# Kernel optimization log

Hardware: AMD Instinct MI355X
Metric: run time of the kernel (lower is better)

Reference implementation:

```python
import jax, jax.numpy as jnp
import numpy as np

N = 100000          # nodes
E = 1600000         # edges (avg degree 16)
IN_F = 256          # in_features
OUT_F = 128         # out_features


def setup_inputs() -> dict:
    key = jax.random.key(0)
    k1, k2, k3, k4, k5 = jax.random.split(key, 5)
    x = jax.random.normal(k1, (N, IN_F), dtype=jnp.float32)
    edge_index = jax.random.randint(k2, (2, E), 0, N, dtype=jnp.int32)
    # xavier_uniform-style init (gain 1.414)
    def xav(k, shape):
        fan_in, fan_out = shape[0], shape[1]
        bound = 1.414 * np.sqrt(6.0 / (fan_in + fan_out))
        return jax.random.uniform(k, shape, jnp.float32, -bound, bound)
    W = xav(k3, (IN_F, OUT_F))
    a = xav(k4, (2 * OUT_F, 1))
    W_em = xav(k5, (IN_F, OUT_F))
    return {"x": x, "edge_index": edge_index, "W": W, "a": a, "W_em": W_em}


def reference(x, edge_index, W, a, W_em):
    # DisGALayer.forward_sparse, att_type=1, gnn_type='AT', eval mode (dropout off)
    src = edge_index[0]
    dst = edge_index[1]
    h = x @ W                                   # [N, OUT_F]
    # edge_e = cat(h[src], h[dst]) @ a  ==  h[src]@a_src + h[dst]@a_dst
    a_src, a_dst = a[:OUT_F], a[OUT_F:]
    edge_e = h[src] @ a_src + h[dst] @ a_dst    # [E, 1]
    edge_ob = jax.nn.sigmoid(edge_e)            # [E, 1]
    # sp_softmax: softmax of edge values grouped by row (src)
    v = jnp.exp(edge_ob - jax.lax.stop_gradient(edge_ob.max()))
    denom = jax.ops.segment_sum(v, src, num_segments=N)   # [N, 1]
    attention = v / denom[src]                  # [E, 1]
    # sp_matmul: h_prime[i] = sum_{e: src(e)=i} att_e * h_em[dst(e)]
    h_em = x @ W_em                             # [N, OUT_F]
    h_prime = jax.ops.segment_sum(attention * h_em[dst], src, num_segments=N)
    return h_prime, edge_e
```

## Files before the change

kernel.cpp:

```cpp
#include <hip/hip_runtime.h>
#include <hip/hip_bf16.h>

#define NN 100000
#define NE 1600000
#define INF 256
#define OUTF 128
#define NBK ((NN + 127) / 128)
#define CHUNK 4096
#define NBA ((NE + CHUNK - 1) / CHUNK)
#define NGRP (NN / 32)
#define SCAP 6144
#define NMM 1563

#define GLOBAL_AS __attribute__((address_space(1)))
#define LDS_AS __attribute__((address_space(3)))

typedef __attribute__((ext_vector_type(8))) short short8;
typedef __attribute__((ext_vector_type(4))) float f32x4;

static __device__ __forceinline__ short f2bf(float f) {
    __hip_bfloat16 h = __float2bfloat16(f);
    return *reinterpret_cast<short*>(&h);
}

__global__ void k_setup(const float* __restrict__ W, const float* __restrict__ a,
                        const float* __restrict__ Wem, const int* __restrict__ src,
                        float* __restrict__ wsv, float* __restrict__ wdv,
                        ushort* __restrict__ Bsw, int* __restrict__ cntA) {
    const int b = blockIdx.x, t = threadIdx.x;
    if (b == 0) {
        const float* Wr = W + (size_t)t * OUTF;
        float sa = 0.f, sb = 0.f;
        #pragma unroll 8
        for (int k = 0; k < OUTF; ++k) {
            float w = Wr[k];
            sa += w * a[k];
            sb += w * a[OUTF + k];
        }
        wsv[t] = sa;
        wdv[t] = sb;
    } else if (b <= 8) {
        const int kt = b - 1;
        for (int idx = t; idx < 4096; idx += 256) {
            const int ct = idx >> 9;
            const int lane = (idx >> 3) & 63;
            const int j = idx & 7;
            const int k = kt * 32 + (lane >> 4) * 8 + j;
            const int c = ct * 16 + (lane & 15);
            Bsw[((size_t)(kt * 8 + ct) * 64 + lane) * 8 + j] =
                (ushort)f2bf(Wem[(size_t)k * OUTF + c]);
        }
    } else {
        __shared__ int cnt[NBK];
        const int c = b - 9;
        const int e0 = c * CHUNK;
        for (int i = t; i < NBK; i += 256) cnt[i] = 0;
        __syncthreads();
        for (int i = t; i < CHUNK; i += 256) {
            const int e = e0 + i;
            if (e < NE) atomicAdd(&cnt[src[e] >> 7], 1);
        }
        __syncthreads();
        for (int i = t; i < NBK; i += 256) cntA[(size_t)c * NBK + i] = cnt[i];
    }
}

__global__ __launch_bounds__(256) void k_mmcs(
    const float* __restrict__ x, const ushort* __restrict__ Bsw,
    const float* __restrict__ wsv, const float* __restrict__ wdv,
    const int* __restrict__ cntA,
    float* __restrict__ s1, float* __restrict__ s2,
    char* __restrict__ hem8, float* __restrict__ scaleA,
    int* __restrict__ baseA, int* __restrict__ bsumB) {
    __shared__ float xs[64 * 256];
    __shared__ int sm[512];
    const int b = blockIdx.x;
    const int t = threadIdx.x;
    if (b < NMM) {
        const int w = t >> 6, lane = t & 63;
        const int rowbase = b * 64 + w * 16;
        const int r0 = lane & 15, kq = lane >> 4;

        #pragma unroll
        for (int it = 0; it < 16; ++it) {
            const int r = w * 16 + it;
            const int gr = b * 64 + r;
            const int grc = (gr < NN) ? gr : NN - 1;
            const int chunk = lane ^ (r & 15);
            const float* gsrc = x + (size_t)grc * INF + chunk * 4;
            __builtin_amdgcn_global_load_lds(
                (const GLOBAL_AS uint*)gsrc,
                (LDS_AS uint*)&xs[r * 256], 16, 0, 0);
        }
        __syncthreads();

        const float* xrow = &xs[(size_t)(w * 16 + r0) * 256];
        const short8* bp = reinterpret_cast<const short8*>(Bsw);
        f32x4 acc[8];
        #pragma unroll
        for (int ct = 0; ct < 8; ++ct) acc[ct] = (f32x4){0.f, 0.f, 0.f, 0.f};
        float sa = 0.f, sb = 0.f;

        #pragma unroll
        for (int kt = 0; kt < 8; ++kt) {
            const int c0 = kt * 8 + kq * 2;
            const float4 a0 = *reinterpret_cast<const float4*>(
                xrow + ((c0 ^ r0) << 2));
            const float4 a1 = *reinterpret_cast<const float4*>(
                xrow + (((c0 + 1) ^ r0) << 2));
            const float4 w0 = *reinterpret_cast<const float4*>(wsv + kt * 32 + kq * 8);
            const float4 w1 = *reinterpret_cast<const float4*>(wsv + kt * 32 + kq * 8 + 4);
            const float4 u0 = *reinterpret_cast<const float4*>(wdv + kt * 32 + kq * 8);
            const float4 u1 = *reinterpret_cast<const float4*>(wdv + kt * 32 + kq * 8 + 4);
            sa += a0.x * w0.x + a0.y * w0.y + a0.z * w0.z + a0.w * w0.w
                + a1.x * w1.x + a1.y * w1.y + a1.z * w1.z + a1.w * w1.w;
            sb += a0.x * u0.x + a0.y * u0.y + a0.z * u0.z + a0.w * u0.w
                + a1.x * u1.x + a1.y * u1.y + a1.z * u1.z + a1.w * u1.w;
            short8 af;
            af[0] = f2bf(a0.x); af[1] = f2bf(a0.y); af[2] = f2bf(a0.z); af[3] = f2bf(a0.w);
            af[4] = f2bf(a1.x); af[5] = f2bf(a1.y); af[6] = f2bf(a1.z); af[7] = f2bf(a1.w);
            #pragma unroll
            for (int ct = 0; ct < 8; ++ct) {
                const short8 bf = bp[(size_t)(kt * 8 + ct) * 64 + lane];
                acc[ct] = __builtin_amdgcn_mfma_f32_16x16x32_bf16(af, bf, acc[ct], 0, 0, 0);
            }
        }

        sa += __shfl_xor(sa, 16); sa += __shfl_xor(sa, 32);
        sb += __shfl_xor(sb, 16); sb += __shfl_xor(sb, 32);
        const int row = rowbase + r0;
        if (kq == 0 && row < NN) { s1[row] = sa; s2[row] = sb; }

        float mx[4];
        #pragma unroll
        for (int i = 0; i < 4; ++i) {
            float m = 0.f;
            #pragma unroll
            for (int ct = 0; ct < 8; ++ct) m = fmaxf(m, fabsf(acc[ct][i]));
            m = fmaxf(m, __shfl_xor(m, 1));
            m = fmaxf(m, __shfl_xor(m, 2));
            m = fmaxf(m, __shfl_xor(m, 4));
            m = fmaxf(m, __shfl_xor(m, 8));
            mx[i] = m;
        }
        #pragma unroll
        for (int i = 0; i < 4; ++i) {
            const int rr = rowbase + kq * 4 + i;
            const float inv = (mx[i] > 0.f) ? 127.f / mx[i] : 0.f;
            if (r0 == 0 && rr < NN) scaleA[rr] = mx[i];
            #pragma unroll
            for (int ct = 0; ct < 8; ++ct) {
                int q = (int)rintf(acc[ct][i] * inv);
                q = (q > 127) ? 127 : ((q < -127) ? -127 : q);
                uint p = (uint)(q & 255);
                p |= ((uint)__shfl_xor((int)p, 1) & 255u) << 8;
                uint word = p | ((uint)__shfl_xor((int)p, 2) << 16);
                if ((r0 & 3) == 0 && rr < NN) {
                    *reinterpret_cast<uint*>(
                        hem8 + ((size_t)(ct >> 1) * NN + rr) * 32
                             + (ct & 1) * 16 + r0) = word;
                }
            }
        }
    } else {
        const int bb = b - NMM;
        const int v0 = (t < NBA) ? cntA[(size_t)t * NBK + bb] : 0;
        const int t2 = t + 256;
        const int v1 = (t2 < NBA) ? cntA[(size_t)t2 * NBK + bb] : 0;
        sm[t] = v0;
        sm[t2] = v1;
        __syncthreads();
        for (int off = 1; off < 512; off <<= 1) {
            const int a0 = (t >= off) ? sm[t - off] : 0;
            const int a1 = (t2 >= off) ? sm[t2 - off] : 0;
            __syncthreads();
            sm[t] += a0;
            sm[t2] += a1;
            __syncthreads();
        }
        if (t < NBA) baseA[(size_t)t * NBK + bb] = sm[t] - v0;
        if (t2 < NBA) baseA[(size_t)t2 * NBK + bb] = sm[t2] - v1;
        if (t == 255) bsumB[bb] = sm[511];
    }
}

__global__ __launch_bounds__(1024) void k_bbase(
    const int* __restrict__ bsumB, int* __restrict__ bbase,
    int* __restrict__ offs) {
    __shared__ int sm[1024];
    const int t = threadIdx.x;
    const int v = (t < NBK) ? bsumB[t] : 0;
    sm[t] = v;
    __syncthreads();
    for (int off = 1; off < 1024; off <<= 1) {
        const int add = (t >= off) ? sm[t - off] : 0;
        __syncthreads();
        sm[t] += add;
        __syncthreads();
    }
    if (t < NBK) bbase[t] = sm[t] - v;
    if (t == 0) { bbase[NBK] = NE; offs[NN] = NE; }
}

__global__ __launch_bounds__(256) void k_binA(
    const int* __restrict__ src, const int* __restrict__ dst,
    const float* __restrict__ s1, const float* __restrict__ s2,
    float* __restrict__ ee_out, const int* __restrict__ bbase,
    const int* __restrict__ baseA, int2* __restrict__ ebA) {
    __shared__ int base[NBK];
    __shared__ int cnt[NBK];
    const int t = threadIdx.x;
    const int c = blockIdx.x;
    const int e0 = c * CHUNK;
    for (int i = t; i < NBK; i += 256) {
        base[i] = bbase[i] + baseA[(size_t)c * NBK + i];
        cnt[i] = 0;
    }
    __syncthreads();
    for (int i = t; i < CHUNK; i += 256) {
        const int e = e0 + i;
        if (e < NE) {
            const int s = src[e], d = dst[e];
            const float ee = s1[s] + s2[d];
            __builtin_nontemporal_store(ee, ee_out + e);
            const float ob = 1.f / (1.f + __expf(-ee));
            const float v = __expf(ob);
            int vq = (int)((v - 1.f) * 16384.f + 0.5f);
            vq = (vq > 32767) ? 32767 : vq;
            const int bk = s >> 7;
            const int r = atomicAdd(&cnt[bk], 1);
            ebA[base[bk] + r] = make_int2((d << 7) | (s & 127), vq);
        }
    }
}

__global__ __launch_bounds__(256) void k_sortB(
    const int* __restrict__ bbase, const int2* __restrict__ ebA,
    const float* __restrict__ scaleA,
    uint* __restrict__ ebB, int* __restrict__ offs) {
    __shared__ uint rx[SCAP];
    __shared__ ushort ry[SCAP];
    __shared__ int cnt[128];
    __shared__ int sum[128];
    __shared__ int sm[128];
    __shared__ int cur[128];
    __shared__ float fsl[128];
    const int b = blockIdx.x, t = threadIdx.x;
    const int n0 = b << 7;
    const int lo = bbase[b];
    const int hi = bbase[b + 1];
    const int n = hi - lo;
    if (t < 128) { cnt[t] = 0; sum[t] = 0; }
    __syncthreads();
    for (int i = t; i < n; i += 256) {
        const int2 r = ebA[lo + i];
        if (i < SCAP) { rx[i] = (uint)r.x; ry[i] = (ushort)r.y; }
        const int sidx = r.x & 127;
        atomicAdd(&cnt[sidx], 1);
        atomicAdd(&sum[sidx], r.y);
    }
    __syncthreads();
    const int v = (t < 128) ? cnt[t] : 0;
    if (t < 128) sm[t] = v;
    __syncthreads();
    for (int off = 1; off < 128; off <<= 1) {
        int add = 0;
        if (t < 128 && t >= off) add = sm[t - off];
        __syncthreads();
        if (t < 128) sm[t] += add;
        __syncthreads();
    }
    if (t < 128) {
        const int excl = sm[t] - v;
        cur[t] = excl;
        const int node = n0 + t;
        if (node < NN) offs[node] = lo + excl;
        fsl[t] = (v > 0) ? 1.f / (float)(v * 16384 + sum[t]) : 0.f;
    }
    __syncthreads();
    for (int i = t; i < n; i += 256) {
        uint x;
        int y;
        if (i < SCAP) { x = rx[i]; y = (int)ry[i]; }
        else { const int2 r = ebA[lo + i]; x = (uint)r.x; y = r.y; }
        const int sidx = x & 127;
        const uint d = x >> 7;
        const float att = (float)(16384 + y) * fsl[sidx];
        const float w = att * scaleA[d];
        int wq = (int)(w * 1024.f + 0.5f);
        wq = (wq > 32767) ? 32767 : wq;
        const int p = atomicAdd(&cur[sidx], 1);
        ebB[lo + p] = (d << 15) | (uint)wq;
    }
}

__global__ __launch_bounds__(256) void k_aggregate(
    const uint* __restrict__ eb, const int* __restrict__ offs,
    const char* __restrict__ hem8, float* __restrict__ out0) {
    const int slice = blockIdx.x & 3;
    const int grp = blockIdx.x >> 2;
    const int t = threadIdx.x;
    const int node = grp * 32 + (t >> 3);
    const int f = t & 7;
    const char* base = hem8 + (size_t)slice * NN * 32 + f * 4;
    const int beg = offs[node];
    const int end = offs[node + 1];

    int a0 = 0, a1 = 0, a2 = 0, a3 = 0;
    int j = beg;
    for (; j + 4 <= end; j += 4) {
        const uint r0 = eb[j];
        const uint r1 = eb[j + 1];
        const uint r2 = eb[j + 2];
        const uint r3 = eb[j + 3];
        const int w0 = (int)(r0 & 0x7fffu);
        const int w1 = (int)(r1 & 0x7fffu);
        const int w2 = (int)(r2 & 0x7fffu);
        const int w3 = (int)(r3 & 0x7fffu);
        const uint u0 = *reinterpret_cast<const uint*>(base + ((size_t)(r0 >> 15)) * 32);
        const uint u1 = *reinterpret_cast<const uint*>(base + ((size_t)(r1 >> 15)) * 32);
        const uint u2 = *reinterpret_cast<const uint*>(base + ((size_t)(r2 >> 15)) * 32);
        const uint u3 = *reinterpret_cast<const uint*>(base + ((size_t)(r3 >> 15)) * 32);
        a0 += w0 * (((int)(u0 << 24)) >> 24) + w1 * (((int)(u1 << 24)) >> 24)
            + w2 * (((int)(u2 << 24)) >> 24) + w3 * (((int)(u3 << 24)) >> 24);
        a1 += w0 * (((int)(u0 << 16)) >> 24) + w1 * (((int)(u1 << 16)) >> 24)
            + w2 * (((int)(u2 << 16)) >> 24) + w3 * (((int)(u3 << 16)) >> 24);
        a2 += w0 * (((int)(u0 << 8)) >> 24) + w1 * (((int)(u1 << 8)) >> 24)
            + w2 * (((int)(u2 << 8)) >> 24) + w3 * (((int)(u3 << 8)) >> 24);
        a3 += w0 * (((int)u0) >> 24) + w1 * (((int)u1) >> 24)
            + w2 * (((int)u2) >> 24) + w3 * (((int)u3) >> 24);
    }
    for (; j < end; ++j) {
        const uint r0 = eb[j];
        const int w0 = (int)(r0 & 0x7fffu);
        const uint u0 = *reinterpret_cast<const uint*>(base + ((size_t)(r0 >> 15)) * 32);
        a0 += w0 * (((int)(u0 << 24)) >> 24);
        a1 += w0 * (((int)(u0 << 16)) >> 24);
        a2 += w0 * (((int)(u0 << 8)) >> 24);
        a3 += w0 * (((int)u0) >> 24);
    }
    const float s = 1.f / (1024.f * 127.f);
    f32x4 o = {a0 * s, a1 * s, a2 * s, a3 * s};
    *reinterpret_cast<f32x4*>(
        out0 + (size_t)node * OUTF + slice * 32 + f * 4) = o;
}

extern "C" void kernel_launch(void* const* d_in, const int* in_sizes, int n_in,
                              void* d_out, int out_size, void* d_ws, size_t ws_size,
                              hipStream_t stream) {
    const float* x   = (const float*)d_in[0];
    const int* eidx  = (const int*)d_in[1];
    const float* W   = (const float*)d_in[2];
    const float* a   = (const float*)d_in[3];
    const float* Wem = (const float*)d_in[4];

    const int* src = eidx;
    const int* dst = eidx + NE;

    float* out0 = (float*)d_out;
    float* out1 = out0 + (size_t)NN * OUTF;

    float* wsv    = (float*)d_ws;
    float* wdv    = wsv + 256;
    float* s1     = wdv + 256;
    float* s2     = s1 + NN;
    float* scaleA = s2 + NN;
    ushort* Bsw   = (ushort*)(scaleA + NN);
    int* offs     = (int*)(Bsw + 32768);
    int* bsumB    = offs + NN + 4;
    int* bbase    = bsumB + 784;
    int* cntA     = bbase + 788;
    int* baseA    = cntA + NBA * NBK;
    int2* ebA     = (int2*)(baseA + NBA * NBK);
    uint* ebB     = (uint*)(ebA + NE);
    char* hem8    = (char*)(ebB + NE);

    hipLaunchKernelGGL(k_setup, dim3(9 + NBA), dim3(256), 0, stream,
                       W, a, Wem, src, wsv, wdv, Bsw, cntA);
    hipLaunchKernelGGL(k_mmcs, dim3(NMM + NBK), dim3(256), 0, stream,
                       x, Bsw, wsv, wdv, cntA, s1, s2, hem8, scaleA,
                       baseA, bsumB);
    hipLaunchKernelGGL(k_bbase, dim3(1), dim3(1024), 0, stream, bsumB, bbase, offs);
    hipLaunchKernelGGL(k_binA, dim3(NBA), dim3(256), 0, stream,
                       src, dst, s1, s2, out1, bbase, baseA, ebA);
    hipLaunchKernelGGL(k_sortB, dim3(NBK), dim3(256), 0, stream,
                       bbase, ebA, scaleA, ebB, offs);
    hipLaunchKernelGGL(k_aggregate, dim3(4 * NGRP), dim3(256), 0, stream,
                       ebB, offs, hem8, out0);
}
```

Measured before the change: 154.6 us.

## Split fused matmul/count-scan kernel; coalesced chunked column scan; per-wave LDS wait

Splits the combined matmul plus count-scan kernel in two. The matmul kernel now uses s_waitcnt instead of a block barrier, since each wave reads only the rows it loaded itself. The count scan moves to a new kernel with 25 blocks that scan 32 bins per block in chunks of 25, which makes the cntA reads coalesced instead of strided. This adds a kernel launch and loses the overlap the fused kernel had between matmul blocks and scan blocks.

```diff
diff --git a/kernel.cpp b/kernel.cpp
--- a/kernel.cpp
+++ b/kernel.cpp
@@ -65,122 +65,131 @@
     }
 }
 
-__global__ __launch_bounds__(256) void k_mmcs(
+__global__ __launch_bounds__(256) void k_mm(
     const float* __restrict__ x, const ushort* __restrict__ Bsw,
     const float* __restrict__ wsv, const float* __restrict__ wdv,
-    const int* __restrict__ cntA,
     float* __restrict__ s1, float* __restrict__ s2,
-    char* __restrict__ hem8, float* __restrict__ scaleA,
-    int* __restrict__ baseA, int* __restrict__ bsumB) {
+    char* __restrict__ hem8, float* __restrict__ scaleA) {
     __shared__ float xs[64 * 256];
-    __shared__ int sm[512];
     const int b = blockIdx.x;
     const int t = threadIdx.x;
-    if (b < NMM) {
-        const int w = t >> 6, lane = t & 63;
-        const int rowbase = b * 64 + w * 16;
-        const int r0 = lane & 15, kq = lane >> 4;
-
+    const int w = t >> 6, lane = t & 63;
+    const int rowbase = b * 64 + w * 16;
+    const int r0 = lane & 15, kq = lane >> 4;
+
+    #pragma unroll
+    for (int it = 0; it < 16; ++it) {
+        const int r = w * 16 + it;
+        const int gr = b * 64 + r;
+        const int grc = (gr < NN) ? gr : NN - 1;
+        const int chunk = lane ^ (r & 15);
+        const float* gsrc = x + (size_t)grc * INF + chunk * 4;
+        __builtin_amdgcn_global_load_lds(
+            (const GLOBAL_AS uint*)gsrc,
+            (LDS_AS uint*)&xs[r * 256], 16, 0, 0);
+    }
+    asm volatile("s_waitcnt vmcnt(0)" ::: "memory");
+
+    const float* xrow = &xs[(size_t)(w * 16 + r0) * 256];
+    const short8* bp = reinterpret_cast<const short8*>(Bsw);
+    f32x4 acc[8];
+    #pragma unroll
+    for (int ct = 0; ct < 8; ++ct) acc[ct] = (f32x4){0.f, 0.f, 0.f, 0.f};
+    float sa = 0.f, sb = 0.f;
+
+    #pragma unroll
+    for (int kt = 0; kt < 8; ++kt) {
+        const int c0 = kt * 8 + kq * 2;
+        const float4 a0 = *reinterpret_cast<const float4*>(
+            xrow + ((c0 ^ r0) << 2));
+        const float4 a1 = *reinterpret_cast<const float4*>(
+            xrow + (((c0 + 1) ^ r0) << 2));
+        const float4 w0 = *reinterpret_cast<const float4*>(wsv + kt * 32 + kq * 8);
+        const float4 w1 = *reinterpret_cast<const float4*>(wsv + kt * 32 + kq * 8 + 4);
+        const float4 u0 = *reinterpret_cast<const float4*>(wdv + kt * 32 + kq * 8);
+        const float4 u1 = *reinterpret_cast<const float4*>(wdv + kt * 32 + kq * 8 + 4);
+        sa += a0.x * w0.x + a0.y * w0.y + a0.z * w0.z + a0.w * w0.w
+            + a1.x * w1.x + a1.y * w1.y + a1.z * w1.z + a1.w * w1.w;
+        sb += a0.x * u0.x + a0.y * u0.y + a0.z * u0.z + a0.w * u0.w
+            + a1.x * u1.x + a1.y * u1.y + a1.z * u1.z + a1.w * u1.w;
+        short8 af;
+        af[0] = f2bf(a0.x); af[1] = f2bf(a0.y); af[2] = f2bf(a0.z); af[3] = f2bf(a0.w);
+        af[4] = f2bf(a1.x); af[5] = f2bf(a1.y); af[6] = f2bf(a1.z); af[7] = f2bf(a1.w);
         #pragma unroll
-        for (int it = 0; it < 16; ++it) {
-            const int r = w * 16 + it;
-            const int gr = b * 64 + r;
-            const int grc = (gr < NN) ? gr : NN - 1;
-            const int chunk = lane ^ (r & 15);
-            const float* gsrc = x + (size_t)grc * INF + chunk * 4;
-            __builtin_amdgcn_global_load_lds(
-                (const GLOBAL_AS uint*)gsrc,
-                (LDS_AS uint*)&xs[r * 256], 16, 0, 0);
-        }
-        __syncthreads();
-
-        const float* xrow = &xs[(size_t)(w * 16 + r0) * 256];
-        const short8* bp = reinterpret_cast<const short8*>(Bsw);
-        f32x4 acc[8];
+        for (int ct = 0; ct < 8; ++ct) {
+            const short8 bf = bp[(size_t)(kt * 8 + ct) * 64 + lane];
+            acc[ct] = __builtin_amdgcn_mfma_f32_16x16x32_bf16(af, bf, acc[ct], 0, 0, 0);
+        }
+    }
+
+    sa += __shfl_xor(sa, 16); sa += __shfl_xor(sa, 32);
+    sb += __shfl_xor(sb, 16); sb += __shfl_xor(sb, 32);
+    const int row = rowbase + r0;
+    if (kq == 0 && row < NN) { s1[row] = sa; s2[row] = sb; }
+
+    float mx[4];
+    #pragma unroll
+    for (int i = 0; i < 4; ++i) {
+        float m = 0.f;
         #pragma unroll
-        for (int ct = 0; ct < 8; ++ct) acc[ct] = (f32x4){0.f, 0.f, 0.f, 0.f};
-        float sa = 0.f, sb = 0.f;
-
+        for (int ct = 0; ct < 8; ++ct) m = fmaxf(m, fabsf(acc[ct][i]));
+        m = fmaxf(m, __shfl_xor(m, 1));
+        m = fmaxf(m, __shfl_xor(m, 2));
+        m = fmaxf(m, __shfl_xor(m, 4));
+        m = fmaxf(m, __shfl_xor(m, 8));
+        mx[i] = m;
+    }
+    #pragma unroll
+    for (int i = 0; i < 4; ++i) {
+        const int rr = rowbase + kq * 4 + i;
+        const float inv = (mx[i] > 0.f) ? 127.f / mx[i] : 0.f;
+        if (r0 == 0 && rr < NN) scaleA[rr] = mx[i];
         #pragma unroll
-        for (int kt = 0; kt < 8; ++kt) {
-            const int c0 = kt * 8 + kq * 2;
-            const float4 a0 = *reinterpret_cast<const float4*>(
-                xrow + ((c0 ^ r0) << 2));
-            const float4 a1 = *reinterpret_cast<const float4*>(
-                xrow + (((c0 + 1) ^ r0) << 2));
-            const float4 w0 = *reinterpret_cast<const float4*>(wsv + kt * 32 + kq * 8);
-            const float4 w1 = *reinterpret_cast<const float4*>(wsv + kt * 32 + kq * 8 + 4);
-            const float4 u0 = *reinterpret_cast<const float4*>(wdv + kt * 32 + kq * 8);
-            const float4 u1 = *reinterpret_cast<const float4*>(wdv + kt * 32 + kq * 8 + 4);
-            sa += a0.x * w0.x + a0.y * w0.y + a0.z * w0.z + a0.w * w0.w
-                + a1.x * w1.x + a1.y * w1.y + a1.z * w1.z + a1.w * w1.w;
-            sb += a0.x * u0.x + a0.y * u0.y + a0.z * u0.z + a0.w * u0.w
-                + a1.x * u1.x + a1.y * u1.y + a1.z * u1.z + a1.w * u1.w;
-            short8 af;
-            af[0] = f2bf(a0.x); af[1] = f2bf(a0.y); af[2] = f2bf(a0.z); af[3] = f2bf(a0.w);
-            af[4] = f2bf(a1.x); af[5] = f2bf(a1.y); af[6] = f2bf(a1.z); af[7] = f2bf(a1.w);
-            #pragma unroll
-            for (int ct = 0; ct < 8; ++ct) {
-                const short8 bf = bp[(size_t)(kt * 8 + ct) * 64 + lane];
-                acc[ct] = __builtin_amdgcn_mfma_f32_16x16x32_bf16(af, bf, acc[ct], 0, 0, 0);
+        for (int ct = 0; ct < 8; ++ct) {
+            int q = (int)rintf(acc[ct][i] * inv);
+            q = (q > 127) ? 127 : ((q < -127) ? -127 : q);
+            uint p = (uint)(q & 255);
+            p |= ((uint)__shfl_xor((int)p, 1) & 255u) << 8;
+            uint word = p | ((uint)__shfl_xor((int)p, 2) << 16);
+            if ((r0 & 3) == 0 && rr < NN) {
+                *reinterpret_cast<uint*>(
+                    hem8 + ((size_t)(ct >> 1) * NN + rr) * 32
+                         + (ct & 1) * 16 + r0) = word;
             }
         }
-
-        sa += __shfl_xor(sa, 16); sa += __shfl_xor(sa, 32);
-        sb += __shfl_xor(sb, 16); sb += __shfl_xor(sb, 32);
-        const int row = rowbase + r0;
-        if (kq == 0 && row < NN) { s1[row] = sa; s2[row] = sb; }
-
-        float mx[4];
-        #pragma unroll
-        for (int i = 0; i < 4; ++i) {
-            float m = 0.f;
-            #pragma unroll
-            for (int ct = 0; ct < 8; ++ct) m = fmaxf(m, fabsf(acc[ct][i]));
-            m = fmaxf(m, __shfl_xor(m, 1));
-            m = fmaxf(m, __shfl_xor(m, 2));
-            m = fmaxf(m, __shfl_xor(m, 4));
-            m = fmaxf(m, __shfl_xor(m, 8));
-            mx[i] = m;
-        }
-        #pragma unroll
-        for (int i = 0; i < 4; ++i) {
-            const int rr = rowbase + kq * 4 + i;
-            const float inv = (mx[i] > 0.f) ? 127.f / mx[i] : 0.f;
-            if (r0 == 0 && rr < NN) scaleA[rr] = mx[i];
-            #pragma unroll
-            for (int ct = 0; ct < 8; ++ct) {
-                int q = (int)rintf(acc[ct][i] * inv);
-                q = (q > 127) ? 127 : ((q < -127) ? -127 : q);
-                uint p = (uint)(q & 255);
-                p |= ((uint)__shfl_xor((int)p, 1) & 255u) << 8;
-                uint word = p | ((uint)__shfl_xor((int)p, 2) << 16);
-                if ((r0 & 3) == 0 && rr < NN) {
-                    *reinterpret_cast<uint*>(
-                        hem8 + ((size_t)(ct >> 1) * NN + rr) * 32
-                             + (ct & 1) * 16 + r0) = word;
-                }
+    }
+}
+
+#define CPS 25
+__global__ __launch_bounds__(512) void k_cscan(
+    const int* __restrict__ cntA, int* __restrict__ baseA,
+    int* __restrict__ bsumB) {
+    __shared__ int ssum[512];
+    const int t = threadIdx.x;
+    const int bo = t & 31, cl = t >> 5;
+    const int b = blockIdx.x * 32 + bo;
+    const bool bok = (b < NBK);
+    int s = 0;
+    if (bok) {
+        for (int i = 0; i < CPS; ++i) {
+            const int c = cl * CPS + i;
+            if (c < NBA) s += cntA[(size_t)c * NBK + b];
+        }
+    }
+    ssum[t] = s;
+    __syncthreads();
+    int base = 0;
+    for (int c2 = 0; c2 < cl; ++c2) base += ssum[c2 * 32 + bo];
+    if (bok && cl == 15) bsumB[b] = base + s;
+    if (bok) {
+        int run = base;
+        for (int i = 0; i < CPS; ++i) {
+            const int c = cl * CPS + i;
+            if (c < NBA) {
+                baseA[(size_t)c * NBK + b] = run;
+                run += cntA[(size_t)c * NBK + b];
             }
         }
-    } else {
-        const int bb = b - NMM;
-        const int v0 = (t < NBA) ? cntA[(size_t)t * NBK + bb] : 0;
-        const int t2 = t + 256;
-        const int v1 = (t2 < NBA) ? cntA[(size_t)t2 * NBK + bb] : 0;
-        sm[t] = v0;
-        sm[t2] = v1;
-        __syncthreads();
-        for (int off = 1; off < 512; off <<= 1) {
-            const int a0 = (t >= off) ? sm[t - off] : 0;
-            const int a1 = (t2 >= off) ? sm[t2 - off] : 0;
-            __syncthreads();
-            sm[t] += a0;
-            sm[t2] += a1;
-            __syncthreads();
-        }
-        if (t < NBA) baseA[(size_t)t * NBK + bb] = sm[t] - v0;
-        if (t2 < NBA) baseA[(size_t)t2 * NBK + bb] = sm[t2] - v1;
-        if (t == 255) bsumB[bb] = sm[511];
     }
 }
 
@@ -377,9 +386,10 @@
 
     hipLaunchKernelGGL(k_setup, dim3(9 + NBA), dim3(256), 0, stream,
                        W, a, Wem, src, wsv, wdv, Bsw, cntA);
-    hipLaunchKernelGGL(k_mmcs, dim3(NMM + NBK), dim3(256), 0, stream,
-                       x, Bsw, wsv, wdv, cntA, s1, s2, hem8, scaleA,
-                       baseA, bsumB);
+    hipLaunchKernelGGL(k_mm, dim3(NMM), dim3(256), 0, stream,
+                       x, Bsw, wsv, wdv, s1, s2, hem8, scaleA);
+    hipLaunchKernelGGL(k_cscan, dim3(25), dim3(512), 0, stream,
+                       cntA, baseA, bsumB);
     hipLaunchKernelGGL(k_bbase, dim3(1), dim3(1024), 0, stream, bsumB, bbase, offs);
     hipLaunchKernelGGL(k_binA, dim3(NBA), dim3(256), 0, stream,
                        src, dst, s1, s2, out1, bbase, baseA, ebA);
```

Measured after the change: 166.5 us. 1.08x slower.
